# Optimization experiments

Measured on AMD Instinct MI355X. Metric: run time of the kernel, lower is better.

Reference implementation:

```python
import jax, jax.numpy as jnp
import numpy as np
import math

D = 4096            # input dim and all hidden dims
TOKENS = (4, 2048)  # batch, seq
P = 0.8             # excitatory fraction for EI layers


def conn_dense(kernel, x):
    # bool kernel interpreted as +1 (True) / -1 (False)
    w = jnp.where(kernel, jnp.asarray(1.0, x.dtype), jnp.asarray(-1.0, x.dtype))
    return x @ w


def ei_dense(x, kernel, scale, p):
    in_dim = x.shape[-1]
    ne = round(in_dim * p)  # excitatory count
    x_exc = x[..., :ne]
    x_inh = x[..., ne:]
    xx = jnp.concatenate([x_exc, (-p / (1.0 - p)) * x_inh], axis=-1)
    return scale * conn_dense(kernel, xx)


def setup_inputs() -> dict:
    key = jax.random.key(0)
    ks = jax.random.split(key, 4)
    x = jax.random.normal(ks[0], (*TOKENS, D), dtype=jnp.float32)
    k0 = jax.random.bernoulli(ks[1], 0.5, (D, D))
    k1 = jax.random.bernoulli(ks[2], 0.5, (D, D))
    k2 = jax.random.bernoulli(ks[3], 0.5, (D, D))
    s = jnp.asarray(1.0 / math.sqrt(D), dtype=jnp.float32)
    return {"x": x, "k0": k0, "s0": s, "k1": k1, "s1": s, "k2": k2, "s2": s}


def reference(x, k0, s0, k1, s1, k2, s2):
    # layer 0: Dense_01 (plain +/-1 matmul, scale), then relu*2
    h = s0 * conn_dense(k0, x)
    h = jax.nn.relu(h) * 2.0
    # layer 1: Dense_EI, then relu*2
    h = ei_dense(h, k1, s1, P)
    h = jax.nn.relu(h) * 2.0
    # layer 2: Dense_EI (no activation on last layer)
    return ei_dense(h, k2, s2, P)
```

## Files before the change

### kernel.cpp

```cpp
#include <hip/hip_runtime.h>
#include <stdint.h>

#define DD 4096
#define NE_IDX 3277

typedef __attribute__((ext_vector_type(8))) short short8;
typedef __attribute__((ext_vector_type(4))) float f32x4;
typedef __attribute__((ext_vector_type(4))) unsigned int u32x4;

__device__ __forceinline__ unsigned short f2bf(float f) {
    unsigned int u = __float_as_uint(f);
    u += 0x7fffu + ((u >> 16) & 1u);
    return (unsigned short)(u >> 16);
}

__device__ __forceinline__ void gload16(const void* g, void* l) {
    __builtin_amdgcn_global_load_lds(
        (const __attribute__((address_space(1))) unsigned int*)g,
        (__attribute__((address_space(3))) unsigned int*)l,
        16, 0, 0);
}

__global__ void detect_kernel(const unsigned int* __restrict__ k0, int* __restrict__ flag) {
    if (blockIdx.x == 0 && threadIdx.x == 0) {
        int ok4 = 1;
        for (int i = 0; i < 256; ++i) {
            unsigned int v = k0[i];
            if (!(v == 0u || v == 1u || v == 0x3f800000u)) { ok4 = 0; break; }
        }
        *flag = ok4;
    }
}

__global__ void pack_x_kernel(const float* __restrict__ x, unsigned short* __restrict__ xb, int n8) {
    const int stride = gridDim.x * blockDim.x;
    for (int i = blockIdx.x * blockDim.x + threadIdx.x; i < n8; i += stride) {
        const float4* p = (const float4*)(x + (size_t)i * 8);
        float4 a = p[0], b = p[1];
        short8 r;
        r[0] = (short)f2bf(a.x); r[1] = (short)f2bf(a.y);
        r[2] = (short)f2bf(a.z); r[3] = (short)f2bf(a.w);
        r[4] = (short)f2bf(b.x); r[5] = (short)f2bf(b.y);
        r[6] = (short)f2bf(b.z); r[7] = (short)f2bf(b.w);
        *(short8*)(xb + (size_t)i * 8) = r;
    }
}

__global__ void pack_w_kernel(const void* __restrict__ kin, unsigned short* __restrict__ wt,
                              const float* __restrict__ sptr, float inh, int ne,
                              const int* __restrict__ flag) {
    __shared__ unsigned short tile[64][68];
    const int elem4 = *flag;
    const float s = *sptr;
    const int i0 = blockIdx.x * 64;
    const int j0 = blockIdx.y * 64;
    const int t = threadIdx.x;
    {
        const int il = t >> 2;
        const int jc = (t & 3) * 16;
        const int gi = i0 + il;
        const float mag = s * ((gi < ne) ? 1.0f : inh);
        const unsigned short pos = f2bf(mag);
        const unsigned short neg = f2bf(-mag);
        if (elem4) {
            const unsigned int* k32 = (const unsigned int*)kin + (size_t)gi * DD + j0 + jc;
            #pragma unroll
            for (int q = 0; q < 4; ++q) {
                u32x4 v = *(const u32x4*)(k32 + q * 4);
                #pragma unroll
                for (int e = 0; e < 4; ++e)
                    tile[il][jc + q * 4 + e] = v[e] ? pos : neg;
            }
        } else {
            const unsigned char* k8 = (const unsigned char*)kin + (size_t)gi * DD + j0 + jc;
            u32x4 v = *(const u32x4*)k8;
            #pragma unroll
            for (int q = 0; q < 4; ++q) {
                unsigned int w = v[q];
                tile[il][jc + q * 4 + 0] = (w & 0xffu) ? pos : neg;
                tile[il][jc + q * 4 + 1] = ((w >> 8) & 0xffu) ? pos : neg;
                tile[il][jc + q * 4 + 2] = ((w >> 16) & 0xffu) ? pos : neg;
                tile[il][jc + q * 4 + 3] = ((w >> 24) & 0xffu) ? pos : neg;
            }
        }
    }
    __syncthreads();
    {
        const int jl = t >> 2;
        const int ic = (t & 3) * 16;
        short8 o0, o1;
        #pragma unroll
        for (int e = 0; e < 8; ++e) o0[e] = (short)tile[ic + e][jl];
        #pragma unroll
        for (int e = 0; e < 8; ++e) o1[e] = (short)tile[ic + 8 + e][jl];
        unsigned short* dst = wt + (size_t)(j0 + jl) * DD + i0 + ic;
        *(short8*)(dst) = o0;
        *(short8*)(dst + 8) = o1;
    }
}

#define PHASE(MH, NH, STAGE_STMT) do {                                          \
    short8 af[2][4], bf[2][2];                                                  \
    _Pragma("unroll")                                                           \
    for (int kk = 0; kk < 2; ++kk) {                                            \
        _Pragma("unroll")                                                       \
        for (int m = 0; m < 4; ++m)                                             \
            af[kk][m] = *(const short8*)(abuf + (abase[(MH)*4+m] ^ ((kk*4+fg)<<4))); \
        _Pragma("unroll")                                                       \
        for (int n = 0; n < 2; ++n)                                             \
            bf[kk][n] = *(const short8*)(bbuf + (bbase[(NH)*2+n] ^ ((kk*4+fg)<<4))); \
    }                                                                           \
    STAGE_STMT;                                                                 \
    __builtin_amdgcn_s_barrier();                                               \
    asm volatile("s_waitcnt lgkmcnt(0)" ::: "memory");                          \
    __builtin_amdgcn_sched_barrier(0);                                          \
    __builtin_amdgcn_s_setprio(1);                                              \
    _Pragma("unroll")                                                           \
    for (int kk = 0; kk < 2; ++kk)                                              \
        _Pragma("unroll")                                                       \
        for (int m = 0; m < 4; ++m)                                             \
            _Pragma("unroll")                                                   \
            for (int n = 0; n < 2; ++n)                                         \
                acc[(MH)*4+m][(NH)*2+n] = __builtin_amdgcn_mfma_f32_16x16x32_bf16( \
                    af[kk][m], bf[kk][n], acc[(MH)*4+m][(NH)*2+n], 0, 0, 0);    \
    __builtin_amdgcn_s_setprio(0);                                              \
    __builtin_amdgcn_sched_barrier(0);                                          \
    asm volatile("s_waitcnt vmcnt(4)" ::: "memory");                            \
    __builtin_amdgcn_s_barrier();                                               \
    __builtin_amdgcn_sched_barrier(0);                                          \
} while (0)

template <int MODE>
__global__ __launch_bounds__(512, 2)
void gemm256_kernel(const unsigned short* __restrict__ A,
                    const unsigned short* __restrict__ Bt,
                    void* __restrict__ Cout)
{
    __shared__ unsigned short L[65536];

    const int tid  = threadIdx.x;
    const int lane = tid & 63;
    const int fr   = lane & 15;
    const int fg   = lane >> 4;
    const int wave = tid >> 6;
    const int wr   = wave >> 2;
    const int wc   = wave & 3;

    int wg = blockIdx.x;
    const int per = gridDim.x >> 3;
    wg = (wg & 7) * per + (wg >> 3);
    const int tm = wg >> 4;
    const int tn = wg & 15;

    const size_t arow0 = (size_t)tm * 256;
    const size_t brow0 = (size_t)tn * 256;

    const int rq = tid >> 3;
    const int wq = (tid >> 6) << 3;
    const int srcoff = (((tid & 7) ^ ((tid >> 3) & 7)) << 3);

    auto stageA = [&](int sb, int c, int kt) {
        #pragma unroll
        for (int q = 0; q < 2; ++q) {
            const int dr = c * 64 + q * 128 + rq;
            gload16(A + ((arow0 + dr) << 12) + kt + srcoff,
                    (void*)&L[sb + ((c * 64 + q * 128 + wq) << 6)]);
        }
    };
    auto stageB = [&](int sb, int c, int kt) {
        #pragma unroll
        for (int q = 0; q < 2; ++q) {
            const int lr  = q * 64 + rq;
            const int dr  = c * 32 + (lr & 31) + (lr >> 5) * 64;
            const int wlr = q * 64 + wq;
            const int wdr = c * 32 + (wlr & 31) + (wlr >> 5) * 64;
            gload16(Bt + ((brow0 + dr) << 12) + kt + srcoff,
                    (void*)&L[sb + 16384 + (wdr << 6)]);
        }
    };

    int abase[8], bbase[4];
    #pragma unroll
    for (int m = 0; m < 8; ++m) {
        const int r = wr * 128 + m * 16 + fr;
        abase[m] = r * 128 + ((r & 7) << 4);
    }
    #pragma unroll
    for (int n = 0; n < 4; ++n) {
        const int r = wc * 64 + n * 16 + fr;
        bbase[n] = r * 128 + ((r & 7) << 4);
    }

    f32x4 acc[8][4];
    #pragma unroll
    for (int m = 0; m < 8; ++m)
        #pragma unroll
        for (int n = 0; n < 4; ++n)
            acc[m][n] = (f32x4){0.f, 0.f, 0.f, 0.f};

    stageA(0, 0, 0); stageB(0, 0, 0); stageB(0, 1, 0); stageA(0, 1, 0);
    asm volatile("s_waitcnt vmcnt(4)" ::: "memory");
    __builtin_amdgcn_s_barrier();
    __builtin_amdgcn_sched_barrier(0);

    for (int t = 0; t < 63; ++t) {
        const char* abuf = (const char*)L + (t & 1) * 65536;
        const char* bbuf = abuf + 32768;
        const int sb  = ((t & 1) ^ 1) * 32768;
        const int kt1 = (t + 1) * 64;
        PHASE(0, 0, stageA(sb, 0, kt1));
        PHASE(0, 1, stageB(sb, 0, kt1));
        PHASE(1, 0, stageB(sb, 1, kt1));
        PHASE(1, 1, stageA(sb, 1, kt1));
    }
    asm volatile("s_waitcnt vmcnt(0)" ::: "memory");
    __builtin_amdgcn_s_barrier();
    __builtin_amdgcn_sched_barrier(0);
    {
        const char* abuf = (const char*)L + 65536;
        const char* bbuf = abuf + 32768;
        PHASE(0, 0, (void)0);
        PHASE(0, 1, (void)0);
        PHASE(1, 0, (void)0);
        PHASE(1, 1, (void)0);
    }

    const int orow0 = tm * 256 + wr * 128;
    const int ocol0 = tn * 256 + wc * 64;
    #pragma unroll
    for (int m = 0; m < 8; ++m) {
        #pragma unroll
        for (int n = 0; n < 4; ++n) {
            #pragma unroll
            for (int j = 0; j < 4; ++j) {
                const int row = orow0 + m * 16 + fg * 4 + j;
                const int col = ocol0 + n * 16 + fr;
                float v = acc[m][n][j];
                if (MODE == 1) {
                    v = fmaxf(v, 0.0f) * 2.0f;
                    ((unsigned short*)Cout)[((size_t)row << 12) + col] = f2bf(v);
                } else {
                    ((float*)Cout)[((size_t)row << 12) + col] = v;
                }
            }
        }
    }
}

extern "C" void kernel_launch(void* const* d_in, const int* in_sizes, int n_in,
                              void* d_out, int out_size, void* d_ws, size_t ws_size,
                              hipStream_t stream) {
    const float* x  = (const float*)d_in[0];
    const void*  k0 = d_in[1];
    const float* s0 = (const float*)d_in[2];
    const void*  k1 = d_in[3];
    const float* s1 = (const float*)d_in[4];
    const void*  k2 = d_in[5];
    const float* s2 = (const float*)d_in[6];

    const int M = in_sizes[0] / DD;

    const size_t act_bytes = (size_t)M * DD * 2;
    const size_t w_bytes   = (size_t)DD * DD * 2;
    const size_t need      = act_bytes * 2 + w_bytes + 256;
    if (ws_size < need) return;

    char* ws = (char*)d_ws;
    unsigned short* xb = (unsigned short*)ws;
    unsigned short* h1 = (unsigned short*)(ws + act_bytes);
    unsigned short* wt = (unsigned short*)(ws + act_bytes * 2);
    int* flag          = (int*)(ws + act_bytes * 2 + w_bytes);

    detect_kernel<<<1, 64, 0, stream>>>((const unsigned int*)k0, flag);
    pack_x_kernel<<<2048, 256, 0, stream>>>(x, xb, M * DD / 8);

    dim3 pw_grid(DD / 64, DD / 64);
    const int gemm_grid = (M / 256) * (DD / 256);

    pack_w_kernel<<<pw_grid, 256, 0, stream>>>(k0, wt, s0, 1.0f, DD, flag);
    gemm256_kernel<1><<<gemm_grid, 512, 0, stream>>>(xb, wt, h1);

    pack_w_kernel<<<pw_grid, 256, 0, stream>>>(k1, wt, s1, -4.0f, NE_IDX, flag);
    gemm256_kernel<1><<<gemm_grid, 512, 0, stream>>>(h1, wt, xb);

    pack_w_kernel<<<pw_grid, 256, 0, stream>>>(k2, wt, s2, -4.0f, NE_IDX, flag);
    gemm256_kernel<0><<<gemm_grid, 512, 0, stream>>>(xb, wt, (float*)d_out);
}
```

Baseline: 855.6 us.

## Reuse fragments across phases with snake order and drop per-phase trailing barrier

The four sub-tile phases now follow a snake order (00,01,11,10), so the A or B fragments from the previous phase stay in registers and only the changed operand is re-read from LDS. The vmcnt wait moves ahead of the first barrier, and the trailing barrier is kept only at the end of each k-iteration, cutting barriers per phase from two to roughly one. LDS buffer offsets are toggled by XOR on precomputed bases instead of being recomputed per iteration. Fewer barriers risk LDS overwrite hazards if the staging ordering is not fully covered, and holding fragments across phases raises register pressure.

```diff
diff --git a/kernel.cpp b/kernel.cpp
--- a/kernel.cpp
+++ b/kernel.cpp
@@ -99,18 +99,23 @@
     }
 }
 
-#define PHASE(MH, NH, STAGE_STMT) do {                                          \
-    short8 af[2][4], bf[2][2];                                                  \
-    _Pragma("unroll")                                                           \
-    for (int kk = 0; kk < 2; ++kk) {                                            \
+#define PHASE(MH, NH, LA, LB, STAGE_STMT, EB) do {                              \
+    if (LA) {                                                                   \
         _Pragma("unroll")                                                       \
-        for (int m = 0; m < 4; ++m)                                             \
-            af[kk][m] = *(const short8*)(abuf + (abase[(MH)*4+m] ^ ((kk*4+fg)<<4))); \
+        for (int m = 0; m < 4; ++m) {                                           \
+            af[0][m] = *(const short8*)(Lc + (ab[(MH)*4+m] ^ kx0));             \
+            af[1][m] = *(const short8*)(Lc + (ab[(MH)*4+m] ^ kx1));             \
+        }                                                                       \
+    }                                                                           \
+    if (LB) {                                                                   \
         _Pragma("unroll")                                                       \
-        for (int n = 0; n < 2; ++n)                                             \
-            bf[kk][n] = *(const short8*)(bbuf + (bbase[(NH)*2+n] ^ ((kk*4+fg)<<4))); \
+        for (int n = 0; n < 2; ++n) {                                           \
+            bf[0][n] = *(const short8*)(Lc + (bb[(NH)*2+n] ^ kx0));             \
+            bf[1][n] = *(const short8*)(Lc + (bb[(NH)*2+n] ^ kx1));             \
+        }                                                                       \
     }                                                                           \
     STAGE_STMT;                                                                 \
+    asm volatile("s_waitcnt vmcnt(4)" ::: "memory");                            \
     __builtin_amdgcn_s_barrier();                                               \
     asm volatile("s_waitcnt lgkmcnt(0)" ::: "memory");                          \
     __builtin_amdgcn_sched_barrier(0);                                          \
@@ -125,9 +130,7 @@
                     af[kk][m], bf[kk][n], acc[(MH)*4+m][(NH)*2+n], 0, 0, 0);    \
     __builtin_amdgcn_s_setprio(0);                                              \
     __builtin_amdgcn_sched_barrier(0);                                          \
-    asm volatile("s_waitcnt vmcnt(4)" ::: "memory");                            \
-    __builtin_amdgcn_s_barrier();                                               \
-    __builtin_amdgcn_sched_barrier(0);                                          \
+    if (EB) __builtin_amdgcn_s_barrier();                                       \
 } while (0)
 
 template <int MODE>
@@ -137,6 +140,7 @@
                     void* __restrict__ Cout)
 {
     __shared__ unsigned short L[65536];
+    const char* Lc = (const char*)L;
 
     const int tid  = threadIdx.x;
     const int lane = tid & 63;
@@ -179,18 +183,21 @@
         }
     };
 
-    int abase[8], bbase[4];
+    const int kx0 = fg << 4;
+    const int kx1 = (4 + fg) << 4;
+    int ab[8], bb[4];
     #pragma unroll
     for (int m = 0; m < 8; ++m) {
         const int r = wr * 128 + m * 16 + fr;
-        abase[m] = r * 128 + ((r & 7) << 4);
+        ab[m] = r * 128 + ((r & 7) << 4);
     }
     #pragma unroll
     for (int n = 0; n < 4; ++n) {
         const int r = wc * 64 + n * 16 + fr;
-        bbase[n] = r * 128 + ((r & 7) << 4);
-    }
-
+        bb[n] = 32768 + r * 128 + ((r & 7) << 4);
+    }
+
+    short8 af[2][4], bf[2][2];
     f32x4 acc[8][4];
     #pragma unroll
     for (int m = 0; m < 8; ++m)
@@ -204,26 +211,24 @@
     __builtin_amdgcn_sched_barrier(0);
 
     for (int t = 0; t < 63; ++t) {
-        const char* abuf = (const char*)L + (t & 1) * 65536;
-        const char* bbuf = abuf + 32768;
         const int sb  = ((t & 1) ^ 1) * 32768;
         const int kt1 = (t + 1) * 64;
-        PHASE(0, 0, stageA(sb, 0, kt1));
-        PHASE(0, 1, stageB(sb, 0, kt1));
-        PHASE(1, 0, stageB(sb, 1, kt1));
-        PHASE(1, 1, stageA(sb, 1, kt1));
+        PHASE(0, 0, 1, 1, stageA(sb, 0, kt1), 0);
+        PHASE(0, 1, 0, 1, stageB(sb, 0, kt1), 0);
+        PHASE(1, 1, 1, 0, stageB(sb, 1, kt1), 0);
+        PHASE(1, 0, 0, 1, stageA(sb, 1, kt1), 1);
+        #pragma unroll
+        for (int i = 0; i < 8; ++i) ab[i] ^= 65536;
+        #pragma unroll
+        for (int i = 0; i < 4; ++i) bb[i] ^= 65536;
     }
     asm volatile("s_waitcnt vmcnt(0)" ::: "memory");
     __builtin_amdgcn_s_barrier();
     __builtin_amdgcn_sched_barrier(0);
-    {
-        const char* abuf = (const char*)L + 65536;
-        const char* bbuf = abuf + 32768;
-        PHASE(0, 0, (void)0);
-        PHASE(0, 1, (void)0);
-        PHASE(1, 0, (void)0);
-        PHASE(1, 1, (void)0);
-    }
+    PHASE(0, 0, 1, 1, (void)0, 0);
+    PHASE(0, 1, 0, 1, (void)0, 0);
+    PHASE(1, 1, 1, 0, (void)0, 0);
+    PHASE(1, 0, 0, 1, (void)0, 0);
 
     const int orow0 = tm * 256 + wr * 128;
     const int ocol0 = tn * 256 + wc * 64;
```

Measured after the change: 711.1 us. 1.2x faster.
